# Kernel optimization log

Hardware: AMD Instinct MI355X
Metric: run time of the kernel (lower is better)

Reference implementation:

```python
import jax, jax.numpy as jnp
import numpy as np

BS, S, DM, H, DK, DV, PRED = 64, 128, 512, 8, 512, 512, 96
NF = S * DM  # Flatten_Head nf = patch_num * d_model
SCALE_INIT = (DM // H) ** (-0.5)  # head_dim from d_model//n_heads per _ScaledDotProductAttention


def setup_inputs() -> dict:
    key = jax.random.key(0)
    ks = jax.random.split(key, 24)
    g = lambda k, shp: (0.02 * jax.random.normal(k, shp)).astype(jnp.float32)
    inp = {
        "x": jax.random.normal(ks[0], (BS, S, DM), dtype=jnp.float32),
        "prev": jax.random.normal(ks[1], (BS, H, S, S), dtype=jnp.float32),
        # multi-head attention projections (d_k = d_v = d_model per TMBlock)
        "Wq": g(ks[2], (DM, H * DK)), "bq": jnp.zeros((H * DK,), jnp.float32),
        "Wk": g(ks[3], (DM, H * DK)), "bk": jnp.zeros((H * DK,), jnp.float32),
        "Wv": g(ks[4], (DM, H * DV)), "bv": jnp.zeros((H * DV,), jnp.float32),
        "Wo": g(ks[5], (H * DV, DM)), "bo": jnp.zeros((DM,), jnp.float32),
        "scale": jnp.float32(SCALE_INIT),
        # InterPatchMixing: Linear(PatchNum, PatchNum) x2
        "Wi1": g(ks[6], (S, S)), "bi1": jnp.zeros((S,), jnp.float32),
        "Wi2": g(ks[7], (S, S)), "bi2": jnp.zeros((S,), jnp.float32),
        # IntraPatchMixing: Linear(PatchEmbedDim, PatchEmbedDim) x2
        "Wt1": g(ks[8], (DM, DM)), "bt1": jnp.zeros((DM,), jnp.float32),
        "Wt2": g(ks[9], (DM, DM)), "bt2": jnp.zeros((DM,), jnp.float32),
        # Flatten_Head (non-individual): Linear(nf, pred_len)
        "Wh": g(ks[10], (NF, PRED)), "bh": jnp.zeros((PRED,), jnp.float32),
    }
    return inp


def reference(x, prev, Wq, bq, Wk, bk, Wv, bv, Wo, bo, scale,
              Wi1, bi1, Wi2, bi2, Wt1, bt1, Wt2, bt2, Wh, bh):
    bs = x.shape[0]
    # projections -> [bs, H, S, d]
    q = (x @ Wq + bq).reshape(bs, S, H, DK).transpose(0, 2, 1, 3)
    k = (x @ Wk + bk).reshape(bs, S, H, DK).transpose(0, 2, 1, 3)
    v = (x @ Wv + bv).reshape(bs, S, H, DV).transpose(0, 2, 1, 3)
    # manual scaled dot-product attention with residual attention bias (Realformer)
    scores = jnp.einsum('bhqd,bhkd->bhqk', q, k) * scale + prev
    attn = jax.nn.softmax(scores, axis=-1)  # dropout is identity at eval
    o = jnp.einsum('bhqk,bhkd->bhqd', attn, v)
    o = o.transpose(0, 2, 1, 3).reshape(bs, S, H * DV)
    o = o @ Wo + bo  # [bs, S, DM]
    # InterPatchMixing over the patch axis (last dim must be PatchNum)
    t = o.transpose(0, 2, 1)  # [bs, DM, S]
    t = jax.nn.relu(t @ Wi1 + bi1) @ Wi2 + bi2
    y = t.transpose(0, 2, 1)  # [bs, S, DM]
    # IntraPatchMixing over embed dim
    z = jax.nn.relu(y @ Wt1 + bt1) @ Wt2 + bt2
    # Flatten_Head: flatten last two dims -> Linear(nf, pred_len)
    out = z.reshape(bs, NF) @ Wh + bh  # [bs, PRED]
    return out
```

## Files before the change

kernel.cpp:

```cpp
#include <hip/hip_runtime.h>
#include <cstdint>
#include <cstddef>

typedef __bf16 bf16_t;
typedef __bf16 bf16x8 __attribute__((ext_vector_type(8)));
typedef __bf16 bf16x4 __attribute__((ext_vector_type(4)));
typedef float  f32x4  __attribute__((ext_vector_type(4)));

#define MFMA(a, b, c) __builtin_amdgcn_mfma_f32_16x16x32_bf16((a), (b), (c), 0, 0, 0)


__global__ __launch_bounds__(256) void k_convert_dual(const float* __restrict__ in,
                                                      bf16_t* __restrict__ xb,
                                                      bf16_t* __restrict__ xT) {
  __shared__ bf16_t tile[32][34];
  int tx = threadIdx.x & 31, ty = threadIdx.x >> 5;
  int c0 = blockIdx.x * 32, r0 = blockIdx.y * 32;
#pragma unroll
  for (int j = 0; j < 4; ++j) {
    int r = r0 + ty + j * 8;
    bf16_t bv = (bf16_t)in[(size_t)r * 512 + c0 + tx];
    xb[(size_t)r * 512 + c0 + tx] = bv;
    tile[ty + j * 8][tx] = bv;
  }
  __syncthreads();
  int b = (r0 + tx) >> 7, s = (r0 + tx) & 127;
#pragma unroll
  for (int j = 0; j < 4; ++j) {
    int i = c0 + ty + j * 8;
    xT[(size_t)b * 65536 + (size_t)i * 128 + s] = tile[tx][ty + j * 8];
  }
}

__global__ __launch_bounds__(256) void k_transpose_convert(const float* __restrict__ in,
                                                           bf16_t* __restrict__ out,
                                                           int R, int C) {
  __shared__ float tile[32][33];
  int tx = threadIdx.x & 31, ty = threadIdx.x >> 5;
  int c0 = blockIdx.x * 32, r0 = blockIdx.y * 32;
#pragma unroll
  for (int j = 0; j < 4; ++j)
    tile[ty + j * 8][tx] = in[(size_t)(r0 + ty + j * 8) * C + c0 + tx];
  __syncthreads();
#pragma unroll
  for (int j = 0; j < 4; ++j)
    out[(size_t)(c0 + ty + j * 8) * R + r0 + tx] = (bf16_t)tile[tx][ty + j * 8];
}

__global__ __launch_bounds__(256) void k_transpose_b16(const bf16_t* __restrict__ in,
                                                       bf16_t* __restrict__ out,
                                                       int R, int C) {
  __shared__ bf16_t tile[32][34];
  size_t base = (size_t)blockIdx.z * R * C;
  int tx = threadIdx.x & 31, ty = threadIdx.x >> 5;
  int c0 = blockIdx.x * 32, r0 = blockIdx.y * 32;
#pragma unroll
  for (int j = 0; j < 4; ++j)
    tile[ty + j * 8][tx] = in[base + (size_t)(r0 + ty + j * 8) * C + c0 + tx];
  __syncthreads();
#pragma unroll
  for (int j = 0; j < 4; ++j)
    out[base + (size_t)(c0 + ty + j * 8) * R + r0 + tx] = tile[tx][ty + j * 8];
}

template <int BMODE>
__global__ __launch_bounds__(256) void k_wprod(const float* __restrict__ Ap,
                                               const float* __restrict__ Bp,
                                               bf16_t* __restrict__ out,
                                               int ldA, int ldB) {
  __shared__ __align__(16) bf16_t As[128 * 68];
  __shared__ __align__(16) bf16_t Bs[128 * 68];
  const int tid = threadIdx.x, lane = tid & 63, wave = tid >> 6;
  const int wr = (wave >> 1) * 64, wc = (wave & 1) * 64;
  const int lr = lane & 15, lk = (lane >> 4) * 8, frow = (lane >> 4) * 4;
  const int m0 = blockIdx.x * 128, n0 = blockIdx.y * 128, h = blockIdx.z;
  const int sr = tid >> 3, sc = (tid & 7) * 8;
  f32x4 acc[4][4] = {};

  for (int kt = 0; kt < 512; kt += 64) {
#pragma unroll
    for (int rr = 0; rr < 4; ++rr) {
      int r = sr + 32 * rr;
      const float* ap = Ap + (size_t)(m0 + r) * ldA + h * 512 + kt + sc;
      bf16x8 av;
#pragma unroll
      for (int e = 0; e < 8; ++e) av[e] = (bf16_t)ap[e];
      *(bf16x8*)(As + r * 68 + sc) = av;
    }
    if (BMODE == 0) {
#pragma unroll
      for (int rr = 0; rr < 4; ++rr) {
        int r = sr + 32 * rr;
        const float* bp = Bp + (size_t)(n0 + r) * ldB + h * 512 + kt + sc;
        bf16x8 bv;
#pragma unroll
        for (int e = 0; e < 8; ++e) bv[e] = (bf16_t)bp[e];
        *(bf16x8*)(Bs + r * 68 + sc) = bv;
      }
    } else {
#pragma unroll
      for (int rr = 0; rr < 8; ++rr) {
        int kr = (tid >> 5) + 8 * rr;
        int nc = (tid & 31) * 4;
        const float* bp = Bp + (size_t)(h * 512 + kt + kr) * ldB + n0 + nc;
        float4 v = *(const float4*)bp;
        Bs[(nc + 0) * 68 + kr] = (bf16_t)v.x;
        Bs[(nc + 1) * 68 + kr] = (bf16_t)v.y;
        Bs[(nc + 2) * 68 + kr] = (bf16_t)v.z;
        Bs[(nc + 3) * 68 + kr] = (bf16_t)v.w;
      }
    }
    __syncthreads();
#pragma unroll
    for (int kk = 0; kk < 2; ++kk) {
      bf16x8 af[4], bfr[4];
#pragma unroll
      for (int i = 0; i < 4; ++i)
        af[i] = *(const bf16x8*)(As + (wr + i * 16 + lr) * 68 + kk * 32 + lk);
#pragma unroll
      for (int j = 0; j < 4; ++j)
        bfr[j] = *(const bf16x8*)(Bs + (wc + j * 16 + lr) * 68 + kk * 32 + lk);
#pragma unroll
      for (int i = 0; i < 4; ++i)
#pragma unroll
        for (int j = 0; j < 4; ++j)
          acc[i][j] = MFMA(af[i], bfr[j], acc[i][j]);
    }
    __syncthreads();
  }
#pragma unroll
  for (int i = 0; i < 4; ++i)
#pragma unroll
    for (int j = 0; j < 4; ++j)
#pragma unroll
      for (int q = 0; q < 4; ++q) {
        int gm = m0 + wr + i * 16 + frow + q;
        int gn = n0 + wc + j * 16 + lr;
        if (BMODE == 0)
          out[(size_t)(h * 512 + gn) * 512 + gm] = (bf16_t)acc[i][j][q];
        else
          out[(size_t)gn * 4096 + h * 512 + gm] = (bf16_t)acc[i][j][q];
      }
}

__global__ __launch_bounds__(256) void k_sbias(const float* __restrict__ Wq,
                                               const float* __restrict__ bk,
                                               const float* __restrict__ Wk,
                                               const float* __restrict__ bq,
                                               float* __restrict__ W1,
                                               float* __restrict__ W2,
                                               float* __restrict__ c) {
  const int lane = threadIdx.x & 63, wave = threadIdx.x >> 6;
  const int i = blockIdx.x * 4 + wave;
  for (int h = 0; h < 8; ++h) {
    float s1 = 0.f, s2 = 0.f;
    for (int d = lane; d < 512; d += 64) {
      s1 += Wq[(size_t)i * 4096 + h * 512 + d] * bk[h * 512 + d];
      s2 += Wk[(size_t)i * 4096 + h * 512 + d] * bq[h * 512 + d];
    }
#pragma unroll
    for (int o = 32; o > 0; o >>= 1) { s1 += __shfl_down(s1, o); s2 += __shfl_down(s2, o); }
    if (lane == 0) { W1[h * 512 + i] = s1; W2[h * 512 + i] = s2; }
  }
  if (blockIdx.x == 0 && wave == 0) {
    for (int h = 0; h < 8; ++h) {
      float cc = 0.f;
      for (int d = lane; d < 512; d += 64) cc += bq[h * 512 + d] * bk[h * 512 + d];
#pragma unroll
      for (int o = 32; o > 0; o >>= 1) cc += __shfl_down(cc, o);
      if (lane == 0) c[h] = cc;
    }
  }
}

__global__ __launch_bounds__(256) void k_cvec1(const float* __restrict__ bv,
                                               const float* __restrict__ Wo,
                                               float* __restrict__ cpart) {
  int cch = blockIdx.x, d = threadIdx.x * 2;
  float ax = 0.f, ay = 0.f;
  for (int n = cch * 128; n < cch * 128 + 128; ++n) {
    float b = bv[n];
    float2 w = *(const float2*)(Wo + (size_t)n * 512 + d);
    ax += b * w.x; ay += b * w.y;
  }
  cpart[(size_t)cch * 512 + d] = ax;
  cpart[(size_t)cch * 512 + d + 1] = ay;
}
__global__ __launch_bounds__(256) void k_cvec2(const float* __restrict__ cpart,
                                               const float* __restrict__ bo,
                                               float* __restrict__ cvec) {
  int d = blockIdx.x * 256 + threadIdx.x;
  float s = bo[d];
  for (int cch = 0; cch < 32; ++cch) s += cpart[(size_t)cch * 512 + d];
  cvec[d] = s;
}

__global__ __launch_bounds__(256, 4) void k_attn4(const bf16_t* __restrict__ xb,
                                                  const bf16_t* __restrict__ xT,
                                                  bf16_t* __restrict__ TU,
                                                  const float* __restrict__ prev,
                                                  const float* __restrict__ scale_p,
                                                  const float* __restrict__ W1,
                                                  const float* __restrict__ W2,
                                                  const float* __restrict__ cb,
                                                  int hg) {
  __shared__ __align__(16) bf16_t Pl[4][16 * 132];
  __shared__ __align__(16) bf16_t Bw[4][16 * 68];
  __shared__ float scr[512];
  __shared__ float T1s[64], T2s[128];
  __shared__ float csh;

  const int tid = threadIdx.x, lane = tid & 63, wave = tid >> 6;
  const int lr = lane & 15, lk = (lane >> 4) * 8, frow = (lane >> 4) * 4;
  const int bid = blockIdx.x;
  const int bx = (bid & 7) * 64 + (bid >> 3);
  const int b = bx >> 3, hp = (bx >> 1) & 3, half = bx & 1;
  const int h = hg * 4 + hp;
  const int row0 = half * 64;
  const bf16_t* xB = xb + (size_t)b * 65536;
  const bf16_t* xTB = xT + (size_t)b * 65536;
  bf16_t* tB = TU + ((size_t)hp * 8192 + b * 128 + row0) * 512;

  {
    int sp = tid >> 1, part = tid & 1;
    const bf16_t* xrow = xB + (size_t)sp * 512 + part * 256;
    const float* w1 = W1 + h * 512 + part * 256;
    const float* w2 = W2 + h * 512 + part * 256;
    float s1 = 0.f, s2 = 0.f;
    for (int i = 0; i < 256; i += 8) {
      bf16x8 xv = *(const bf16x8*)(xrow + i);
#pragma unroll
      for (int e = 0; e < 8; ++e) {
        float f = (float)xv[e];
        s1 += f * w1[i + e];
        s2 += f * w2[i + e];
      }
    }
    scr[tid] = s1;
    if (tid == 0) csh = cb[h];
    __syncthreads();
    if (tid < 128) {
      float t1v = scr[2 * tid] + scr[2 * tid + 1];
      if (tid >= row0 && tid < row0 + 64) T1s[tid - row0] = t1v;
    }
    __syncthreads();
    scr[tid] = s2;
    __syncthreads();
    if (tid < 128) T2s[tid] = scr[2 * tid] + scr[2 * tid + 1];
    __syncthreads();
  }

  f32x4 sacc[8] = {};
  const bf16_t* aP = tB + (size_t)(wave * 16 + lr) * 512 + lk;
  {
#pragma unroll 2
    for (int kt = 0; kt < 8; ++kt) {
#pragma unroll
      for (int kk = 0; kk < 2; ++kk) {
        bf16x8 af = *(const bf16x8*)(aP + kt * 64 + kk * 32);
        bf16x8 bfr[8];
#pragma unroll
        for (int j = 0; j < 8; ++j)
          bfr[j] = *(const bf16x8*)(xB + (size_t)(j * 16 + lr) * 512 + kt * 64 + kk * 32 + lk);
#pragma unroll
        for (int j = 0; j < 8; ++j) sacc[j] = MFMA(af, bfr[j], sacc[j]);
      }
    }
  }

  const float scl = scale_p[0];
  bf16_t* Plw = Pl[wave];
#pragma unroll
  for (int e = 0; e < 4; ++e) {
    const int rl = wave * 16 + frow + e;
    const float* prow = prev + (((size_t)(b * 8 + h)) * 128 + row0 + rl) * 128;
    float mx = -3.4e38f;
#pragma unroll
    for (int j = 0; j < 8; ++j) {
      int col = j * 16 + lr;
      float v = scl * (sacc[j][e] + T1s[rl] + T2s[col] + csh) + prow[col];
      sacc[j][e] = v;
      mx = fmaxf(mx, v);
    }
    mx = fmaxf(mx, __shfl_xor(mx, 1));
    mx = fmaxf(mx, __shfl_xor(mx, 2));
    mx = fmaxf(mx, __shfl_xor(mx, 4));
    mx = fmaxf(mx, __shfl_xor(mx, 8));
    float sum = 0.f;
#pragma unroll
    for (int j = 0; j < 8; ++j) {
      float p = __expf(sacc[j][e] - mx);
      sacc[j][e] = p;
      sum += p;
    }
    sum += __shfl_xor(sum, 1);
    sum += __shfl_xor(sum, 2);
    sum += __shfl_xor(sum, 4);
    sum += __shfl_xor(sum, 8);
    float inv = 1.f / sum;
#pragma unroll
    for (int j = 0; j < 8; ++j)
      Plw[(frow + e) * 132 + j * 16 + lr] = (bf16_t)(sacc[j][e] * inv);
  }

  bf16_t* Bww = Bw[wave];
#pragma unroll 2
  for (int dc = 0; dc < 8; ++dc) {
    f32x4 oacc[4] = {};
#pragma unroll
    for (int kk = 0; kk < 4; ++kk) {
      bf16x8 pa = *(const bf16x8*)(Plw + lr * 132 + kk * 32 + lk);
      bf16x8 xtf[4];
#pragma unroll
      for (int j = 0; j < 4; ++j)
        xtf[j] = *(const bf16x8*)(xTB + (size_t)(dc * 64 + j * 16 + lr) * 128 + kk * 32 + lk);
#pragma unroll
      for (int j = 0; j < 4; ++j) oacc[j] = MFMA(pa, xtf[j], oacc[j]);
    }
#pragma unroll
    for (int j = 0; j < 4; ++j)
#pragma unroll
      for (int e = 0; e < 4; ++e)
        Bww[(frow + e) * 68 + j * 16 + lr] = (bf16_t)oacc[j][e];
#pragma unroll
    for (int r2 = 0; r2 < 2; ++r2) {
      int row = lane >> 2, chunk = (lane & 3) + r2 * 4;
      *(bf16x8*)(tB + (size_t)(wave * 16 + row) * 512 + dc * 64 + chunk * 8) =
          *(const bf16x8*)(Bww + row * 68 + chunk * 8);
    }
  }
}

template <int OUTMODE, int RELU>
__global__ __launch_bounds__(256) void k_gemm(const bf16_t* __restrict__ A,
                                              const bf16_t* __restrict__ Bt,
                                              const float* __restrict__ bias,
                                              bf16_t* __restrict__ C,
                                              int M, int N, int K) {
  __shared__ __align__(16) bf16_t As[128 * 68];
  __shared__ __align__(16) bf16_t Bs[128 * 68];
  const int tid = threadIdx.x, lane = tid & 63, wave = tid >> 6;
  const int wr = (wave >> 1) * 64, wc = (wave & 1) * 64;
  const int m0 = blockIdx.x * 128, n0 = blockIdx.y * 128;
  const int lr = lane & 15, lk = (lane >> 4) * 8, frow = (lane >> 4) * 4;
  const int sr = tid >> 3, sc = (tid & 7) * 8;
  f32x4 acc[4][4] = {};

  for (int kt = 0; kt < K; kt += 64) {
#pragma unroll
    for (int i = 0; i < 4; ++i) {
      int r = i * 32 + sr;
      *(bf16x8*)(As + r * 68 + sc) = *(const bf16x8*)(A + (size_t)(m0 + r) * K + kt + sc);
      *(bf16x8*)(Bs + r * 68 + sc) = *(const bf16x8*)(Bt + (size_t)(n0 + r) * K + kt + sc);
    }
    __syncthreads();
#pragma unroll
    for (int kk = 0; kk < 2; ++kk) {
      bf16x8 af[4], bfr[4];
#pragma unroll
      for (int i = 0; i < 4; ++i)
        af[i] = *(const bf16x8*)(As + (wr + i * 16 + lr) * 68 + kk * 32 + lk);
#pragma unroll
      for (int j = 0; j < 4; ++j)
        bfr[j] = *(const bf16x8*)(Bs + (wc + j * 16 + lr) * 68 + kk * 32 + lk);
#pragma unroll
      for (int i = 0; i < 4; ++i)
#pragma unroll
        for (int j = 0; j < 4; ++j)
          acc[i][j] = MFMA(af[i], bfr[j], acc[i][j]);
    }
    __syncthreads();
  }
#pragma unroll
  for (int j = 0; j < 4; ++j) {
    int gn = n0 + wc + j * 16 + lr;
    float bv = bias ? bias[gn] : 0.0f;
#pragma unroll
    for (int i = 0; i < 4; ++i) {
#pragma unroll
      for (int q = 0; q < 4; ++q) {
        int gm = m0 + wr + i * 16 + frow + q;
        float v = acc[i][j][q] + bv;
        if (RELU) v = v > 0.0f ? v : 0.0f;
        if (OUTMODE == 0)
          C[(size_t)gm * N + gn] = (bf16_t)v;
        else
          C[((size_t)(gn >> 9) * 8192 + gm) * 512 + (gn & 511)] = (bf16_t)v;
      }
    }
  }
}

template <int MODE>
__global__ __launch_bounds__(256) void k_gemm2(const bf16_t* __restrict__ U,
                                               const bf16_t* __restrict__ bt2,
                                               float* __restrict__ o1acc,
                                               const float* __restrict__ cvec,
                                               bf16_t* __restrict__ o1b, int g) {
  __shared__ __align__(16) bf16_t As[128 * 68];
  __shared__ __align__(16) bf16_t Bs[128 * 68];
  const int tid = threadIdx.x, lane = tid & 63, wave = tid >> 6;
  const int wr = (wave >> 1) * 64, wc = (wave & 1) * 64;
  const int m0 = blockIdx.x * 128, n0 = blockIdx.y * 128;
  const int lr = lane & 15, lk = (lane >> 4) * 8, frow = (lane >> 4) * 4;
  const int sr = tid >> 3, sc = (tid & 7) * 8;
  f32x4 acc[4][4] = {};

  for (int kt = 0; kt < 2048; kt += 64) {
    const int slab = kt >> 9, off = kt & 511;
#pragma unroll
    for (int i = 0; i < 4; ++i) {
      int r = i * 32 + sr;
      *(bf16x8*)(As + r * 68 + sc) =
          *(const bf16x8*)(U + ((size_t)slab * 8192 + m0 + r) * 512 + off + sc);
      *(bf16x8*)(Bs + r * 68 + sc) =
          *(const bf16x8*)(bt2 + (size_t)(n0 + r) * 4096 + g * 2048 + kt + sc);
    }
    __syncthreads();
#pragma unroll
    for (int kk = 0; kk < 2; ++kk) {
      bf16x8 af[4], bfr[4];
#pragma unroll
      for (int i = 0; i < 4; ++i)
        af[i] = *(const bf16x8*)(As + (wr + i * 16 + lr) * 68 + kk * 32 + lk);
#pragma unroll
      for (int j = 0; j < 4; ++j)
        bfr[j] = *(const bf16x8*)(Bs + (wc + j * 16 + lr) * 68 + kk * 32 + lk);
#pragma unroll
      for (int i = 0; i < 4; ++i)
#pragma unroll
        for (int j = 0; j < 4; ++j)
          acc[i][j] = MFMA(af[i], bfr[j], acc[i][j]);
    }
    __syncthreads();
  }
#pragma unroll
  for (int j = 0; j < 4; ++j) {
    int gn = n0 + wc + j * 16 + lr;
#pragma unroll
    for (int i = 0; i < 4; ++i) {
#pragma unroll
      for (int q = 0; q < 4; ++q) {
        int gm = m0 + wr + i * 16 + frow + q;
        size_t idx = (size_t)gm * 512 + gn;
        if (MODE == 0)
          o1acc[idx] = acc[i][j][q];
        else
          o1b[idx] = (bf16_t)(acc[i][j][q] + o1acc[idx] + cvec[gn]);
      }
    }
  }
}

__global__ __launch_bounds__(256) void k_head_partial(const bf16_t* __restrict__ Z,
                                                      const bf16_t* __restrict__ WhT,
                                                      float* __restrict__ part) {
  __shared__ __align__(16) bf16_t As[64 * 68];
  __shared__ __align__(16) bf16_t Bs[96 * 68];
  const int tid = threadIdx.x, lane = tid & 63, wave = tid >> 6;
  const int wr = (wave >> 1) * 32, wc = (wave & 1) * 48;
  const int lr = lane & 15, lk = (lane >> 4) * 8, frow = (lane >> 4) * 4;
  const int k0 = blockIdx.x * 512;
  const int sr = tid >> 3, sc = (tid & 7) * 8;
  f32x4 acc[2][3] = {};
  for (int kt = 0; kt < 512; kt += 64) {
#pragma unroll
    for (int i = 0; i < 2; ++i) {
      int r = i * 32 + sr;
      *(bf16x8*)(As + r * 68 + sc) = *(const bf16x8*)(Z + (size_t)r * 65536 + k0 + kt + sc);
    }
#pragma unroll
    for (int i = 0; i < 3; ++i) {
      int r = i * 32 + sr;
      *(bf16x8*)(Bs + r * 68 + sc) = *(const bf16x8*)(WhT + (size_t)r * 65536 + k0 + kt + sc);
    }
    __syncthreads();
#pragma unroll
    for (int kk = 0; kk < 2; ++kk) {
      bf16x8 af[2], bfr[3];
#pragma unroll
      for (int i = 0; i < 2; ++i)
        af[i] = *(const bf16x8*)(As + (wr + i * 16 + lr) * 68 + kk * 32 + lk);
#pragma unroll
      for (int j = 0; j < 3; ++j)
        bfr[j] = *(const bf16x8*)(Bs + (wc + j * 16 + lr) * 68 + kk * 32 + lk);
#pragma unroll
      for (int i = 0; i < 2; ++i)
#pragma unroll
        for (int j = 0; j < 3; ++j)
          acc[i][j] = MFMA(af[i], bfr[j], acc[i][j]);
    }
    __syncthreads();
  }
#pragma unroll
  for (int i = 0; i < 2; ++i)
#pragma unroll
    for (int j = 0; j < 3; ++j)
#pragma unroll
      for (int q = 0; q < 4; ++q) {
        int m = wr + i * 16 + frow + q;
        int n = wc + j * 16 + lr;
        part[(size_t)blockIdx.x * 6144 + m * 96 + n] = acc[i][j][q];
      }
}

__global__ __launch_bounds__(256) void k_head_reduce(const float* __restrict__ part,
                                                     const float* __restrict__ bias,
                                                     float* __restrict__ out) {
  int idx = blockIdx.x * 256 + threadIdx.x;
  if (idx >= 6144) return;
  float s = bias[idx % 96];
  for (int kb = 0; kb < 128; ++kb) s += part[(size_t)kb * 6144 + idx];
  out[idx] = s;
}

__global__ void k_sentinel(float* out, int n, float val) {
  int i = blockIdx.x * 256 + threadIdx.x;
  if (i < n) out[i] = val;
}

extern "C" void kernel_launch(void* const* d_in, const int* in_sizes, int n_in,
                              void* d_out, int out_size, void* d_ws, size_t ws_size,
                              hipStream_t stream) {
  const float* x    = (const float*)d_in[0];
  const float* prev = (const float*)d_in[1];
  const float* Wq = (const float*)d_in[2];   const float* bq = (const float*)d_in[3];
  const float* Wk = (const float*)d_in[4];   const float* bk = (const float*)d_in[5];
  const float* Wv = (const float*)d_in[6];   const float* bv = (const float*)d_in[7];
  const float* Wo = (const float*)d_in[8];   const float* bo = (const float*)d_in[9];
  const float* scale = (const float*)d_in[10];
  const float* Wi1 = (const float*)d_in[11]; const float* bi1 = (const float*)d_in[12];
  const float* Wi2 = (const float*)d_in[13]; const float* bi2 = (const float*)d_in[14];
  const float* Wt1 = (const float*)d_in[15]; const float* bt1w = (const float*)d_in[16];
  const float* Wt2 = (const float*)d_in[17]; const float* bt2w = (const float*)d_in[18];
  const float* Wh = (const float*)d_in[19];  const float* bh = (const float*)d_in[20];
  float* out = (float*)d_out;

  char* p = (char*)d_ws;
  auto carve = [&](size_t bytes) {
    char* r = p;
    p += (bytes + 255) & ~(size_t)255;
    return r;
  };
  bf16_t* xb    = (bf16_t*)carve((size_t)8192 * 512 * 2);
  bf16_t* xTo1b = (bf16_t*)carve((size_t)8192 * 512 * 2);
  float*  o1acc = (float*)carve((size_t)8192 * 512 * 4);
  bf16_t* bt1   = (bf16_t*)carve((size_t)4096 * 512 * 2);
  bf16_t* bt2   = (bf16_t*)carve((size_t)512 * 4096 * 2);
  float*  W1    = (float*)carve(8 * 512 * 4);
  float*  W2    = (float*)carve(8 * 512 * 4);
  float*  cb    = (float*)carve(8 * 4);
  float*  cvec  = (float*)carve(512 * 4);
  char*   arena = carve((size_t)8192 * 2048 * 2);
  bf16_t* TU    = (bf16_t*)arena;
  float*  cpart = (float*)arena;
  bf16_t* xT    = xTo1b;
  bf16_t* o1b   = xTo1b;
  char* q2 = arena;
  auto carve2 = [&](size_t bytes) {
    char* r = q2;
    q2 += (bytes + 255) & ~(size_t)255;
    return r;
  };
  bf16_t* whT  = (bf16_t*)carve2((size_t)96 * 65536 * 2);
  bf16_t* wt1T = (bf16_t*)carve2((size_t)512 * 512 * 2);
  bf16_t* wt2T = (bf16_t*)carve2((size_t)512 * 512 * 2);
  bf16_t* wi1T = (bf16_t*)carve2((size_t)128 * 128 * 2);
  bf16_t* wi2T = (bf16_t*)carve2((size_t)128 * 128 * 2);
  float*  hp   = (float*)carve2((size_t)128 * 64 * 96 * 4);
  bf16_t* bufB = (bf16_t*)carve2((size_t)8192 * 512 * 2);

  if ((size_t)(p - (char*)d_ws) > ws_size) {
    k_sentinel<<<24, 256, 0, stream>>>(out, 6144, (float)ws_size);
    return;
  }

  dim3 blk(256);
  k_cvec1<<<32, blk, 0, stream>>>(bv, Wo, cpart);
  k_cvec2<<<2, blk, 0, stream>>>(cpart, bo, cvec);
  k_convert_dual<<<dim3(16, 256), blk, 0, stream>>>(x, xb, xT);
  k_wprod<0><<<dim3(4, 4, 8), blk, 0, stream>>>(Wq, Wk, bt1, 4096, 4096);
  k_wprod<1><<<dim3(4, 4, 8), blk, 0, stream>>>(Wv, Wo, bt2, 4096, 512);
  k_sbias<<<128, blk, 0, stream>>>(Wq, bk, Wk, bq, W1, W2, cb);

  k_gemm<2, 0><<<dim3(64, 16), blk, 0, stream>>>(xb, bt1, nullptr, TU, 8192, 2048, 512);
  k_attn4<<<512, blk, 0, stream>>>(xb, xT, TU, prev, scale, W1, W2, cb, 0);
  k_gemm2<0><<<dim3(64, 4), blk, 0, stream>>>(TU, bt2, o1acc, cvec, o1b, 0);
  k_gemm<2, 0><<<dim3(64, 16), blk, 0, stream>>>(xb, bt1 + (size_t)2048 * 512, nullptr, TU,
                                                 8192, 2048, 512);
  k_attn4<<<512, blk, 0, stream>>>(xb, xT, TU, prev, scale, W1, W2, cb, 1);
  k_gemm2<1><<<dim3(64, 4), blk, 0, stream>>>(TU, bt2, o1acc, cvec, o1b, 1);

  k_transpose_convert<<<dim3(4, 4), blk, 0, stream>>>(Wi1, wi1T, 128, 128);
  k_transpose_convert<<<dim3(4, 4), blk, 0, stream>>>(Wi2, wi2T, 128, 128);
  k_transpose_convert<<<dim3(16, 16), blk, 0, stream>>>(Wt1, wt1T, 512, 512);
  k_transpose_convert<<<dim3(16, 16), blk, 0, stream>>>(Wt2, wt2T, 512, 512);
  k_transpose_convert<<<dim3(3, 2048), blk, 0, stream>>>(Wh, whT, 65536, 96);

  k_transpose_b16<<<dim3(16, 4, 64), blk, 0, stream>>>(o1b, bufB, 128, 512);
  k_gemm<0, 1><<<dim3(256, 1), blk, 0, stream>>>(bufB, wi1T, bi1, o1b, 32768, 128, 128);
  k_gemm<0, 0><<<dim3(256, 1), blk, 0, stream>>>(o1b, wi2T, bi2, bufB, 32768, 128, 128);
  k_transpose_b16<<<dim3(4, 16, 64), blk, 0, stream>>>(bufB, o1b, 512, 128);

  k_gemm<0, 1><<<dim3(64, 4), blk, 0, stream>>>(o1b, wt1T, bt1w, bufB, 8192, 512, 512);
  k_gemm<0, 0><<<dim3(64, 4), blk, 0, stream>>>(bufB, wt2T, bt2w, o1b, 8192, 512, 512);

  k_head_partial<<<128, blk, 0, stream>>>(o1b, whT, hp);
  k_head_reduce<<<24, blk, 0, stream>>>(hp, bh, out);
}
```

Before: 496.0 us.

## Precompute attention bias vectors once and split attention into single-wave blocks

A new kernel computes the per-row bias terms T1 and T2 (x dotted with W1 and W2, plus cb) once for all rows and heads. The results are stored in scratch space aliased onto the already-consumed first half of bt1. The attention kernel no longer recomputes these dot products redundantly in every block. It is restructured into 64-thread single-wave blocks, each handling 16 query rows, with four times as many blocks and no block-level barriers. It also raises wave priority around the MFMA loops, at the cost of more blocks and less sharing of the x tile loads across waves.

New measurement: 481.1 us. -3.0%, faster.

```diff
diff --git a/kernel.cpp b/kernel.cpp
--- a/kernel.cpp
+++ b/kernel.cpp
@@ -173,6 +173,46 @@
   }
 }
 
+__global__ __launch_bounds__(256) void k_tbias(const bf16_t* __restrict__ xb,
+                                               const float* __restrict__ W1,
+                                               const float* __restrict__ W2,
+                                               const float* __restrict__ cb,
+                                               float* __restrict__ TallT) {
+  __shared__ float Ws[16][512];
+  __shared__ float scr[128][32];
+  const int tid = threadIdx.x;
+  for (int i = tid; i < 4096; i += 256) {
+    Ws[i >> 9][i & 511] = W1[i];
+    Ws[8 + (i >> 9)][i & 511] = W2[i];
+  }
+  __syncthreads();
+  const int rl = tid & 127, part = tid >> 7;
+  const int row = blockIdx.x * 128 + rl;
+  const bf16_t* xr = xb + (size_t)row * 512 + part * 256;
+  float acc[16] = {};
+  for (int i = 0; i < 256; i += 8) {
+    bf16x8 xv = *(const bf16x8*)(xr + i);
+#pragma unroll
+    for (int e = 0; e < 8; ++e) {
+      float f = (float)xv[e];
+#pragma unroll
+      for (int cI = 0; cI < 16; ++cI) acc[cI] += f * Ws[cI][part * 256 + i + e];
+    }
+  }
+#pragma unroll
+  for (int cI = 0; cI < 16; ++cI) scr[rl][part * 16 + cI] = acc[cI];
+  __syncthreads();
+  if (tid < 128) {
+    int r = blockIdx.x * 128 + tid;
+#pragma unroll
+    for (int cI = 0; cI < 16; ++cI) {
+      float v = scr[tid][cI] + scr[tid][16 + cI];
+      if (cI < 8) v += cb[cI];
+      TallT[cI * 8192 + r] = v;
+    }
+  }
+}
+
 __global__ __launch_bounds__(256) void k_cvec1(const float* __restrict__ bv,
                                                const float* __restrict__ Wo,
                                                float* __restrict__ cpart) {
@@ -195,90 +235,58 @@
   cvec[d] = s;
 }
 
-__global__ __launch_bounds__(256, 4) void k_attn4(const bf16_t* __restrict__ xb,
-                                                  const bf16_t* __restrict__ xT,
-                                                  bf16_t* __restrict__ TU,
-                                                  const float* __restrict__ prev,
-                                                  const float* __restrict__ scale_p,
-                                                  const float* __restrict__ W1,
-                                                  const float* __restrict__ W2,
-                                                  const float* __restrict__ cb,
-                                                  int hg) {
-  __shared__ __align__(16) bf16_t Pl[4][16 * 132];
-  __shared__ __align__(16) bf16_t Bw[4][16 * 68];
-  __shared__ float scr[512];
-  __shared__ float T1s[64], T2s[128];
-  __shared__ float csh;
-
-  const int tid = threadIdx.x, lane = tid & 63, wave = tid >> 6;
+__global__ __launch_bounds__(64, 2) void k_attn5(const bf16_t* __restrict__ xb,
+                                                 const bf16_t* __restrict__ xT,
+                                                 bf16_t* __restrict__ TU,
+                                                 const float* __restrict__ prev,
+                                                 const float* __restrict__ scale_p,
+                                                 const float* __restrict__ TallT,
+                                                 int hg) {
+  __shared__ __align__(16) bf16_t Pl[16 * 136];
+  __shared__ __align__(16) bf16_t Bw[16 * 72];
+
+  const int lane = threadIdx.x;
   const int lr = lane & 15, lk = (lane >> 4) * 8, frow = (lane >> 4) * 4;
   const int bid = blockIdx.x;
-  const int bx = (bid & 7) * 64 + (bid >> 3);
-  const int b = bx >> 3, hp = (bx >> 1) & 3, half = bx & 1;
+  const int bx = (bid & 7) * 256 + (bid >> 3);
+  const int b = bx >> 5, hp = (bx >> 3) & 3, rg = bx & 7;
   const int h = hg * 4 + hp;
-  const int row0 = half * 64;
+  const int r0 = rg * 16;
   const bf16_t* xB = xb + (size_t)b * 65536;
   const bf16_t* xTB = xT + (size_t)b * 65536;
-  bf16_t* tB = TU + ((size_t)hp * 8192 + b * 128 + row0) * 512;
-
-  {
-    int sp = tid >> 1, part = tid & 1;
-    const bf16_t* xrow = xB + (size_t)sp * 512 + part * 256;
-    const float* w1 = W1 + h * 512 + part * 256;
-    const float* w2 = W2 + h * 512 + part * 256;
-    float s1 = 0.f, s2 = 0.f;
-    for (int i = 0; i < 256; i += 8) {
-      bf16x8 xv = *(const bf16x8*)(xrow + i);
-#pragma unroll
-      for (int e = 0; e < 8; ++e) {
-        float f = (float)xv[e];
-        s1 += f * w1[i + e];
-        s2 += f * w2[i + e];
-      }
-    }
-    scr[tid] = s1;
-    if (tid == 0) csh = cb[h];
-    __syncthreads();
-    if (tid < 128) {
-      float t1v = scr[2 * tid] + scr[2 * tid + 1];
-      if (tid >= row0 && tid < row0 + 64) T1s[tid - row0] = t1v;
-    }
-    __syncthreads();
-    scr[tid] = s2;
-    __syncthreads();
-    if (tid < 128) T2s[tid] = scr[2 * tid] + scr[2 * tid + 1];
-    __syncthreads();
-  }
+  bf16_t* tB = TU + ((size_t)hp * 8192 + b * 128 + r0) * 512;
 
   f32x4 sacc[8] = {};
-  const bf16_t* aP = tB + (size_t)(wave * 16 + lr) * 512 + lk;
-  {
-#pragma unroll 2
-    for (int kt = 0; kt < 8; ++kt) {
-#pragma unroll
-      for (int kk = 0; kk < 2; ++kk) {
-        bf16x8 af = *(const bf16x8*)(aP + kt * 64 + kk * 32);
-        bf16x8 bfr[8];
-#pragma unroll
-        for (int j = 0; j < 8; ++j)
-          bfr[j] = *(const bf16x8*)(xB + (size_t)(j * 16 + lr) * 512 + kt * 64 + kk * 32 + lk);
-#pragma unroll
-        for (int j = 0; j < 8; ++j) sacc[j] = MFMA(af, bfr[j], sacc[j]);
-      }
-    }
-  }
+  const bf16_t* aP = tB + (size_t)lr * 512 + lk;
+  const bf16_t* bP = xB + (size_t)lr * 512 + lk;
+  __builtin_amdgcn_s_setprio(1);
+#pragma unroll
+  for (int kx = 0; kx < 16; ++kx) {
+    bf16x8 af = *(const bf16x8*)(aP + kx * 32);
+    bf16x8 bfr[8];
+#pragma unroll
+    for (int j = 0; j < 8; ++j)
+      bfr[j] = *(const bf16x8*)(bP + (size_t)j * 8192 + kx * 32);
+#pragma unroll
+    for (int j = 0; j < 8; ++j) sacc[j] = MFMA(af, bfr[j], sacc[j]);
+  }
+  __builtin_amdgcn_s_setprio(0);
 
   const float scl = scale_p[0];
-  bf16_t* Plw = Pl[wave];
+  const float* t1p = TallT + h * 8192 + b * 128 + r0;
+  const float* t2p = TallT + (8 + h) * 8192 + b * 128;
+  float t2r[8];
+#pragma unroll
+  for (int j = 0; j < 8; ++j) t2r[j] = t2p[j * 16 + lr];
 #pragma unroll
   for (int e = 0; e < 4; ++e) {
-    const int rl = wave * 16 + frow + e;
-    const float* prow = prev + (((size_t)(b * 8 + h)) * 128 + row0 + rl) * 128;
+    const int rl = frow + e;
+    const float t1 = t1p[rl];
+    const float* prow = prev + (((size_t)(b * 8 + h)) * 128 + r0 + rl) * 128;
     float mx = -3.4e38f;
 #pragma unroll
     for (int j = 0; j < 8; ++j) {
-      int col = j * 16 + lr;
-      float v = scl * (sacc[j][e] + T1s[rl] + T2s[col] + csh) + prow[col];
+      float v = scl * (sacc[j][e] + t1 + t2r[j]) + prow[j * 16 + lr];
       sacc[j][e] = v;
       mx = fmaxf(mx, v);
     }
@@ -300,33 +308,34 @@
     float inv = 1.f / sum;
 #pragma unroll
     for (int j = 0; j < 8; ++j)
-      Plw[(frow + e) * 132 + j * 16 + lr] = (bf16_t)(sacc[j][e] * inv);
-  }
-
-  bf16_t* Bww = Bw[wave];
-#pragma unroll 2
+      Pl[rl * 136 + j * 16 + lr] = (bf16_t)(sacc[j][e] * inv);
+  }
+
+#pragma unroll
   for (int dc = 0; dc < 8; ++dc) {
     f32x4 oacc[4] = {};
+    __builtin_amdgcn_s_setprio(1);
 #pragma unroll
     for (int kk = 0; kk < 4; ++kk) {
-      bf16x8 pa = *(const bf16x8*)(Plw + lr * 132 + kk * 32 + lk);
-      bf16x8 xtf[4];
+      bf16x8 pa = *(const bf16x8*)(Pl + lr * 136 + kk * 32 + lk);
+      bf16x8 xf[4];
 #pragma unroll
       for (int j = 0; j < 4; ++j)
-        xtf[j] = *(const bf16x8*)(xTB + (size_t)(dc * 64 + j * 16 + lr) * 128 + kk * 32 + lk);
-#pragma unroll
-      for (int j = 0; j < 4; ++j) oacc[j] = MFMA(pa, xtf[j], oacc[j]);
-    }
+        xf[j] = *(const bf16x8*)(xTB + (size_t)(dc * 64 + j * 16 + lr) * 128 + kk * 32 + lk);
+#pragma unroll
+      for (int j = 0; j < 4; ++j) oacc[j] = MFMA(pa, xf[j], oacc[j]);
+    }
+    __builtin_amdgcn_s_setprio(0);
 #pragma unroll
     for (int j = 0; j < 4; ++j)
 #pragma unroll
       for (int e = 0; e < 4; ++e)
-        Bww[(frow + e) * 68 + j * 16 + lr] = (bf16_t)oacc[j][e];
+        Bw[(frow + e) * 72 + j * 16 + lr] = (bf16_t)oacc[j][e];
 #pragma unroll
     for (int r2 = 0; r2 < 2; ++r2) {
       int row = lane >> 2, chunk = (lane & 3) + r2 * 4;
-      *(bf16x8*)(tB + (size_t)(wave * 16 + row) * 512 + dc * 64 + chunk * 8) =
-          *(const bf16x8*)(Bww + row * 68 + chunk * 8);
+      *(bf16x8*)(tB + (size_t)row * 512 + dc * 64 + chunk * 8) =
+          *(const bf16x8*)(Bw + row * 72 + chunk * 8);
     }
   }
 }
@@ -556,6 +565,7 @@
   float*  cpart = (float*)arena;
   bf16_t* xT    = xTo1b;
   bf16_t* o1b   = xTo1b;
+  float*  TallT = (float*)bt1;
   char* q2 = arena;
   auto carve2 = [&](size_t bytes) {
     char* r = q2;
@@ -584,11 +594,12 @@
   k_sbias<<<128, blk, 0, stream>>>(Wq, bk, Wk, bq, W1, W2, cb);
 
   k_gemm<2, 0><<<dim3(64, 16), blk, 0, stream>>>(xb, bt1, nullptr, TU, 8192, 2048, 512);
-  k_attn4<<<512, blk, 0, stream>>>(xb, xT, TU, prev, scale, W1, W2, cb, 0);
+  k_tbias<<<64, blk, 0, stream>>>(xb, W1, W2, cb, TallT);
+  k_attn5<<<2048, dim3(64), 0, stream>>>(xb, xT, TU, prev, scale, TallT, 0);
   k_gemm2<0><<<dim3(64, 4), blk, 0, stream>>>(TU, bt2, o1acc, cvec, o1b, 0);
   k_gemm<2, 0><<<dim3(64, 16), blk, 0, stream>>>(xb, bt1 + (size_t)2048 * 512, nullptr, TU,
                                                  8192, 2048, 512);
-  k_attn4<<<512, blk, 0, stream>>>(xb, xT, TU, prev, scale, W1, W2, cb, 1);
+  k_attn5<<<2048, dim3(64), 0, stream>>>(xb, xT, TU, prev, scale, TallT, 1);
   k_gemm2<1><<<dim3(64, 4), blk, 0, stream>>>(TU, bt2, o1acc, cvec, o1b, 1);
 
   k_transpose_convert<<<dim3(4, 4), blk, 0, stream>>>(Wi1, wi1T, 128, 128);
```
